# Optimization experiments

Hardware: AMD Instinct MI355X
Metric: run time of the kernel (lower is better)

The kernel has to match this reference:

```python
import jax, jax.numpy as jnp
import numpy as np

T, B, D, H, L = 512, 64, 1024, 1024, 2
W_SCALE = 0.02  # keep tanh out of saturation


def setup_inputs() -> dict:
    key = jax.random.key(0)
    ks = jax.random.split(key, 7)
    return {
        "x": jax.random.normal(ks[0], (T, B, D), dtype=jnp.float32),
        "Wi": jax.random.normal(ks[1], (L, H, D), dtype=jnp.float32) * W_SCALE,
        "bi": jax.random.normal(ks[2], (L, H), dtype=jnp.float32) * W_SCALE,
        "Wh": jax.random.normal(ks[3], (L, H, H), dtype=jnp.float32) * W_SCALE,
        "bh": jax.random.normal(ks[4], (L, H), dtype=jnp.float32) * W_SCALE,
        "Wo": jax.random.normal(ks[5], (L, H, H), dtype=jnp.float32) * W_SCALE,
        "bo": jax.random.normal(ks[6], (L, H), dtype=jnp.float32) * W_SCALE,
    }


def reference(x, Wi, bi, Wh, bh, Wo, bo):
    # Faithful to the original: ONE hidden state shared across all layers,
    # overwritten by each RNNCell call within a timestep.
    num_layers = Wi.shape[0]
    batch = x.shape[1]
    hidden0 = jnp.zeros((batch, Wh.shape[-1]), dtype=x.dtype)

    def step(hidden, xt):
        out = xt
        for l in range(num_layers):
            # h = i2h(out) + h2h(hidden); o = h2o(h); new hidden = tanh(h)
            h = out @ Wi[l].T + bi[l] + hidden @ Wh[l].T + bh[l]  # [B,H]
            out = h @ Wo[l].T + bo[l]
            hidden = jnp.tanh(h)
        return hidden, out

    final_hidden, outs = jax.lax.scan(step, hidden0, x)  # outs: [T,B,H]
    return outs, final_hidden
```

## Files before the change

### kernel.cpp

```cpp
#include <hip/hip_runtime.h>
#include <cstdint>
#include <cstddef>

#define TT   512
#define NWG  256
#define SLOT 65536
#define SLOTB 262144
#define FINALOFF ((size_t)TT * (size_t)SLOT)

#define OFF_M     0
#define OFF_H0    2097152
#define OFF_H1    (OFF_H0 + 131072)
#define OFF_C1    (OFF_H1 + 131072)
#define OFF_FLAGS (OFF_C1 + 4096)

typedef _Float16 f16;
typedef unsigned long long ull;
typedef _Float16 v8h __attribute__((ext_vector_type(8)));
typedef float v4f __attribute__((ext_vector_type(4)));

union U2 { ull u[2]; v8h v; };

__device__ __forceinline__ void st8(void* p, ull v) {
  __hip_atomic_store((ull*)p, v, __ATOMIC_RELAXED, __HIP_MEMORY_SCOPE_AGENT);
}
__device__ __forceinline__ ull ld8(const void* p) {
  return __hip_atomic_load((const ull*)p, __ATOMIC_RELAXED, __HIP_MEMORY_SCOPE_AGENT);
}

__device__ __forceinline__ float rcpf(float x) {
#if __has_builtin(__builtin_amdgcn_rcpf)
  return __builtin_amdgcn_rcpf(x);
#else
  return 1.0f / x;
#endif
}
__device__ __forceinline__ float tanhfast(float x) {
  x = fminf(fmaxf(x, -20.0f), 20.0f);
  const float u = __expf(-2.0f * x);
  return 1.0f - 2.0f * u * rcpf(1.0f + u);
}
__device__ __forceinline__ v8h tanh8(v8h h) {
  v8h r;
#pragma unroll
  for (int i = 0; i < 8; ++i) r[i] = (f16)tanhfast((float)h[i]);
  return r;
}

__global__ void k_init(unsigned int* flags) {
  flags[threadIdx.x] = 0u;
}

__global__ void k_bias_c1(const float* __restrict__ Wi, const float* __restrict__ bi,
                          const float* __restrict__ bh, const float* __restrict__ bo,
                          float* __restrict__ c1) {
  const int i = blockIdx.x * 256 + threadIdx.x;
  const float* row = Wi + 1048576 + (size_t)i * 1024;
  float s = 0.f;
  for (int k = 0; k < 1024; k += 4) {
    const float4 w = *(const float4*)&row[k];
    const float4 v = *(const float4*)&bo[k];
    s += w.x * v.x + w.y * v.y + w.z * v.z + w.w * v.w;
  }
  c1[i] = s + bi[1024 + i] + bh[1024 + i];
}

__global__ __launch_bounds__(256) void k_gemm_M(const float* __restrict__ Wi,
                                                const float* __restrict__ Wo,
                                                f16* __restrict__ Mh) {
  const float* A = Wi + 1048576;
  const float* B = Wo;
  __shared__ float As[16][68];
  __shared__ float Bs[16][68];
  const int bi = blockIdx.x >> 4, bj = blockIdx.x & 15;
  const int i0 = bi * 64, d0 = bj * 64;
  const int ti = threadIdx.x >> 4, tj = threadIdx.x & 15;
  float acc[4][4] = {};
  for (int kc = 0; kc < 1024; kc += 16) {
    const int r = threadIdx.x >> 2, cg = (threadIdx.x & 3) << 2;
    const float4 av = *(const float4*)&A[(size_t)(i0 + r) * 1024 + kc + cg];
    As[cg + 0][r] = av.x; As[cg + 1][r] = av.y; As[cg + 2][r] = av.z; As[cg + 3][r] = av.w;
    const int c2 = threadIdx.x >> 4, dg = (threadIdx.x & 15) << 2;
    const float4 bv = *(const float4*)&B[(size_t)(kc + c2) * 1024 + d0 + dg];
    *(float4*)&Bs[c2][dg] = bv;
    __syncthreads();
#pragma unroll
    for (int kk = 0; kk < 16; ++kk) {
      float a[4], b[4];
#pragma unroll
      for (int q = 0; q < 4; ++q) { a[q] = As[kk][ti * 4 + q]; b[q] = Bs[kk][tj * 4 + q]; }
#pragma unroll
      for (int p = 0; p < 4; ++p)
#pragma unroll
        for (int q = 0; q < 4; ++q) acc[p][q] += a[p] * b[q];
    }
    __syncthreads();
  }
#pragma unroll
  for (int p = 0; p < 4; ++p)
#pragma unroll
    for (int q = 0; q < 4; ++q)
      Mh[(size_t)(i0 + ti * 4 + p) * 1024 + (size_t)(d0 + tj * 4 + q)] = (f16)acc[p][q];
}

__global__ void k_convert_x(const float* __restrict__ x, float* __restrict__ dout) {
  const size_t idx4 = (size_t)blockIdx.x * 256 + threadIdx.x;
  const int t = (int)(idx4 >> 14);
  const int r = (int)(idx4 & 16383);
  const float4 v = ((const float4*)x)[idx4];
  f16* dst = (f16*)((char*)dout + (size_t)t * SLOTB + 131072) + (size_t)r * 4;
  dst[0] = (f16)v.x; dst[1] = (f16)v.y; dst[2] = (f16)v.z; dst[3] = (f16)v.w;
}

__global__ __launch_bounds__(256) void k_z1(const float* __restrict__ Wi,
                                            const float* __restrict__ bi,
                                            const float* __restrict__ bh,
                                            float* __restrict__ dout) {
  const int t = blockIdx.x >> 4, jt = blockIdx.x & 15;
  const int tid = threadIdx.x, l = tid & 63, w = tid >> 6;
  const int lj = l & 15, lk = l >> 4;
  const int jrow = jt * 64 + w * 16 + lj;
  const f16* xh = (const f16*)((const char*)dout + (size_t)t * SLOTB + 131072);
  v4f acc[4] = {{0.f,0.f,0.f,0.f},{0.f,0.f,0.f,0.f},{0.f,0.f,0.f,0.f},{0.f,0.f,0.f,0.f}};
  const float* wrow = Wi + (size_t)jrow * 1024;
  for (int ks = 0; ks < 32; ++ks) {
    const int k0 = ks * 32 + lk * 8;
    const float4 wa = *(const float4*)&wrow[k0];
    const float4 wb = *(const float4*)&wrow[k0 + 4];
    const v8h bf = {(f16)wa.x,(f16)wa.y,(f16)wa.z,(f16)wa.w,
                    (f16)wb.x,(f16)wb.y,(f16)wb.z,(f16)wb.w};
#pragma unroll
    for (int bt = 0; bt < 4; ++bt) {
      const v8h af = *(const v8h*)&xh[(size_t)(bt * 16 + lj) * 1024 + k0];
      acc[bt] = __builtin_amdgcn_mfma_f32_16x16x32_f16(af, bf, acc[bt], 0, 0, 0);
    }
  }
  const float bias = bi[jrow] + bh[jrow];
  f16* z = (f16*)((char*)dout + (size_t)t * SLOTB);
#pragma unroll
  for (int bt = 0; bt < 4; ++bt)
#pragma unroll
    for (int q = 0; q < 4; ++q)
      z[(size_t)(bt * 16 + lk * 4 + q) * 1024 + jrow] = (f16)(acc[bt][q] + bias);
}

__device__ __forceinline__ void gbar_arrive(unsigned int* flags, int wg, unsigned int ph) {
  asm volatile("s_waitcnt vmcnt(0)" ::: "memory");
  __syncthreads();
  if (threadIdx.x == 0)
    __hip_atomic_store(&flags[wg], ph, __ATOMIC_RELAXED, __HIP_MEMORY_SCOPE_AGENT);
}
__device__ __forceinline__ void gbar_wait(unsigned int* flags, unsigned int* gen,
                                          int wg, unsigned int ph) {
  if (wg == 0) {
    const int tt = threadIdx.x;
    if (tt > 0 && tt < NWG)
      while (__hip_atomic_load(&flags[tt], __ATOMIC_RELAXED, __HIP_MEMORY_SCOPE_AGENT) < ph)
        __builtin_amdgcn_s_sleep(1);
    __syncthreads();
    if (tt == 0)
      __hip_atomic_store(gen, ph, __ATOMIC_RELAXED, __HIP_MEMORY_SCOPE_AGENT);
  } else {
    if (threadIdx.x == 0)
      while (__hip_atomic_load(gen, __ATOMIC_RELAXED, __HIP_MEMORY_SCOPE_AGENT) < ph)
        __builtin_amdgcn_s_sleep(1);
    __syncthreads();
  }
  asm volatile("" ::: "memory");
}

__global__ __launch_bounds__(256, 1) void k_rnn(
    const float* __restrict__ Wh, const float* __restrict__ Wo,
    const float* __restrict__ bo,
    char* __restrict__ ws, float* __restrict__ dout)
{
  const f16* Mh = (const f16*)(ws + OFF_M);
  f16* h0h = (f16*)(ws + OFF_H0);
  f16* h1h = (f16*)(ws + OFF_H1);
  const float* c1p = (const float*)(ws + OFF_C1);
  unsigned int* flags = (unsigned int*)(ws + OFF_FLAGS);
  unsigned int* gen = flags + 320;

  const int wg = blockIdx.x;
  const int bq = wg & 3;
  const int jt = wg >> 2;
  const int j0 = jt * 16;
  const int tid = threadIdx.x;
  const int l = tid & 63, w = tid >> 6;
  const int lj = l & 15, lk = l >> 4;
  const int jrow = j0 + lj;

  __shared__ float red[1024];
  __shared__ f16 trh[256];
  __shared__ float trf[256];

  v8h wWh0[8], wM[8], wWh1[8], wWo1[8];
#pragma unroll
  for (int s = 0; s < 8; ++s) {
    const int k0 = w * 256 + s * 32 + lk * 8;
    {
      const float* p = &Wh[(size_t)jrow * 1024 + k0];
      float4 a = *(const float4*)p, b = *(const float4*)(p + 4);
      wWh0[s] = (v8h){(f16)a.x,(f16)a.y,(f16)a.z,(f16)a.w,(f16)b.x,(f16)b.y,(f16)b.z,(f16)b.w};
    }
    {
      const float* p = &Wh[1048576 + (size_t)jrow * 1024 + k0];
      float4 a = *(const float4*)p, b = *(const float4*)(p + 4);
      wWh1[s] = (v8h){(f16)a.x,(f16)a.y,(f16)a.z,(f16)a.w,(f16)b.x,(f16)b.y,(f16)b.z,(f16)b.w};
    }
    {
      const float* p = &Wo[1048576 + (size_t)jrow * 1024 + k0];
      float4 a = *(const float4*)p, b = *(const float4*)(p + 4);
      wWo1[s] = (v8h){(f16)a.x,(f16)a.y,(f16)a.z,(f16)a.w,(f16)b.x,(f16)b.y,(f16)b.z,(f16)b.w};
    }
    wM[s] = *(const v8h*)&Mh[(size_t)jrow * 1024 + k0];
  }
  const int rb = tid >> 4, rj = tid & 15;
  const float c1v = c1p[j0 + rj];
  const float bo1v = bo[1024 + j0 + rj];

  const size_t actbase = (size_t)(bq * 16 + lj) * 1024 + (size_t)(w * 256 + lk * 8);
  unsigned int ph = 0;

  for (int t = 0; t <= TT; ++t) {
    const bool A = (t < TT), R = (t > 0);
    v8h hraw[8];

    if (R) {
      ull u0[8], u1[8];
#pragma unroll
      for (int s = 0; s < 8; ++s) {
        const f16* p = h1h + actbase + s * 32;
        u0[s] = ld8(p); u1[s] = ld8(p + 4);
      }
#pragma unroll
      for (int s = 0; s < 8; ++s) { U2 c; c.u[0] = u0[s]; c.u[1] = u1[s]; hraw[s] = c.v; }
    }

    if (A) {
      v4f acc = {0.f, 0.f, 0.f, 0.f};
      if (R) {
#pragma unroll
        for (int s = 0; s < 8; ++s)
          acc = __builtin_amdgcn_mfma_f32_16x16x32_f16(tanh8(hraw[s]), wWh0[s], acc, 0, 0, 0);
      }
#pragma unroll
      for (int q = 0; q < 4; ++q) red[w * 256 + (lk * 4 + q) * 16 + lj] = acc[q];
      __syncthreads();
      float h0 = red[tid] + red[256 + tid] + red[512 + tid] + red[768 + tid];
      const f16* z1 = (const f16*)((const char*)dout + (size_t)t * SLOTB);
      h0 += (float)z1[(size_t)(bq * 16 + rb) * 1024 + j0 + rj];
      trh[tid] = (f16)h0;
      __syncthreads();
      if (tid < 64)
        st8(&h0h[(size_t)(bq * 16 + (tid >> 2)) * 1024 + j0 + (tid & 3) * 4],
            ((const ull*)trh)[tid]);
    }
    gbar_arrive(flags, wg, ++ph);

    if (R) {
      v4f a2 = {0.f, 0.f, 0.f, 0.f};
#pragma unroll
      for (int s = 0; s < 8; ++s)
        a2 = __builtin_amdgcn_mfma_f32_16x16x32_f16(hraw[s], wWo1[s], a2, 0, 0, 0);
#pragma unroll
      for (int q = 0; q < 4; ++q) red[w * 256 + (lk * 4 + q) * 16 + lj] = a2[q];
      __syncthreads();
      trf[tid] = red[tid] + red[256 + tid] + red[512 + tid] + red[768 + tid] + bo1v;
      __syncthreads();
      if (tid < 128)
        st8(&dout[(size_t)(t - 1) * SLOT + (size_t)(bq * 16 + (tid >> 3)) * 1024 + j0 + (tid & 7) * 2],
            ((const ull*)trf)[tid]);
    }
    gbar_wait(flags, gen, wg, ph);

    if (A) {
      ull g0[8], g1[8];
#pragma unroll
      for (int s = 0; s < 8; ++s) {
        const f16* p = h0h + actbase + s * 32;
        g0[s] = ld8(p); g1[s] = ld8(p + 4);
      }
      v4f aM = {0.f, 0.f, 0.f, 0.f}, aW = {0.f, 0.f, 0.f, 0.f};
#pragma unroll
      for (int s = 0; s < 8; ++s) {
        U2 c; c.u[0] = g0[s]; c.u[1] = g1[s];
        const v8h gv = c.v;
        aM = __builtin_amdgcn_mfma_f32_16x16x32_f16(gv, wM[s], aM, 0, 0, 0);
        aW = __builtin_amdgcn_mfma_f32_16x16x32_f16(tanh8(gv), wWh1[s], aW, 0, 0, 0);
      }
#pragma unroll
      for (int q = 0; q < 4; ++q) red[w * 256 + (lk * 4 + q) * 16 + lj] = aM[q] + aW[q];
      __syncthreads();
      const float h1 = red[tid] + red[256 + tid] + red[512 + tid] + red[768 + tid] + c1v;
      trh[tid] = (f16)h1;
      const bool last = (t == TT - 1);
      if (last) trf[tid] = tanhfast(h1);
      __syncthreads();
      if (tid < 64)
        st8(&h1h[(size_t)(bq * 16 + (tid >> 2)) * 1024 + j0 + (tid & 3) * 4],
            ((const ull*)trh)[tid]);
      if (last && tid < 128)
        st8(&dout[FINALOFF + (size_t)(bq * 16 + (tid >> 3)) * 1024 + j0 + (tid & 7) * 2],
            ((const ull*)trf)[tid]);
      gbar_arrive(flags, wg, ++ph);
      gbar_wait(flags, gen, wg, ph);
    }
  }
}

extern "C" void kernel_launch(void* const* d_in, const int* in_sizes, int n_in,
                              void* d_out, int out_size, void* d_ws, size_t ws_size,
                              hipStream_t stream) {
  (void)in_sizes; (void)n_in; (void)out_size; (void)ws_size;
  const float* x  = (const float*)d_in[0];
  const float* Wi = (const float*)d_in[1];
  const float* bi = (const float*)d_in[2];
  const float* Wh = (const float*)d_in[3];
  const float* bh = (const float*)d_in[4];
  const float* Wo = (const float*)d_in[5];
  const float* bo = (const float*)d_in[6];
  char* ws = (char*)d_ws;
  float* out = (float*)d_out;

  k_init<<<1, 512, 0, stream>>>((unsigned int*)(ws + OFF_FLAGS));
  k_convert_x<<<32768, 256, 0, stream>>>(x, out);
  k_bias_c1<<<4, 256, 0, stream>>>(Wi, bi, bh, bo, (float*)(ws + OFF_C1));
  k_gemm_M<<<256, 256, 0, stream>>>(Wi, Wo, (f16*)(ws + OFF_M));
  k_z1<<<8192, 256, 0, stream>>>(Wi, bi, bh, out);
  k_rnn<<<NWG, 256, 0, stream>>>(Wh, Wo, bo, ws, out);
}
```

Baseline: 6.034 ms.

## Fuse layer-0 input projection into persistent RNN kernel and localize barriers

Removes the separate x conversion and z1 GEMM kernels. Each workgroup now caches its Wi slice in LDS as fp16 and computes the next timestep's input projection while waiting at the barrier. The global barrier changes from one master workgroup gathering all flags to independent 64-workgroup groups per batch quarter, each polling its peers directly. Tanh of each hidden state is computed once by its producer and stored alongside it, so consumers no longer recompute tanh8. The cost is extra LDS, extra global stores per step, and more barrier polling traffic.

```diff
diff --git a/kernel.cpp b/kernel.cpp
--- a/kernel.cpp
+++ b/kernel.cpp
@@ -5,13 +5,15 @@
 #define TT   512
 #define NWG  256
 #define SLOT 65536
-#define SLOTB 262144
 #define FINALOFF ((size_t)TT * (size_t)SLOT)
 
 #define OFF_M     0
 #define OFF_H0    2097152
-#define OFF_H1    (OFF_H0 + 131072)
-#define OFF_C1    (OFF_H1 + 131072)
+#define OFF_TH0   (OFF_H0 + 131072)
+#define OFF_H1    (OFF_TH0 + 131072)
+#define OFF_TH1   (OFF_H1 + 131072)
+#define OFF_B0    (OFF_TH1 + 131072)
+#define OFF_C1    (OFF_B0 + 4096)
 #define OFF_FLAGS (OFF_C1 + 4096)
 
 typedef _Float16 f16;
@@ -40,20 +42,14 @@
   const float u = __expf(-2.0f * x);
   return 1.0f - 2.0f * u * rcpf(1.0f + u);
 }
-__device__ __forceinline__ v8h tanh8(v8h h) {
-  v8h r;
-#pragma unroll
-  for (int i = 0; i < 8; ++i) r[i] = (f16)tanhfast((float)h[i]);
-  return r;
-}
 
 __global__ void k_init(unsigned int* flags) {
   flags[threadIdx.x] = 0u;
 }
 
-__global__ void k_bias_c1(const float* __restrict__ Wi, const float* __restrict__ bi,
-                          const float* __restrict__ bh, const float* __restrict__ bo,
-                          float* __restrict__ c1) {
+__global__ void k_bias(const float* __restrict__ Wi, const float* __restrict__ bi,
+                       const float* __restrict__ bh, const float* __restrict__ bo,
+                       float* __restrict__ b0, float* __restrict__ c1) {
   const int i = blockIdx.x * 256 + threadIdx.x;
   const float* row = Wi + 1048576 + (size_t)i * 1024;
   float s = 0.f;
@@ -63,6 +59,7 @@
     s += w.x * v.x + w.y * v.y + w.z * v.z + w.w * v.w;
   }
   c1[i] = s + bi[1024 + i] + bh[1024 + i];
+  b0[i] = bi[i] + bh[i];
 }
 
 __global__ __launch_bounds__(256) void k_gemm_M(const float* __restrict__ Wi,
@@ -103,83 +100,42 @@
       Mh[(size_t)(i0 + ti * 4 + p) * 1024 + (size_t)(d0 + tj * 4 + q)] = (f16)acc[p][q];
 }
 
-__global__ void k_convert_x(const float* __restrict__ x, float* __restrict__ dout) {
-  const size_t idx4 = (size_t)blockIdx.x * 256 + threadIdx.x;
-  const int t = (int)(idx4 >> 14);
-  const int r = (int)(idx4 & 16383);
-  const float4 v = ((const float4*)x)[idx4];
-  f16* dst = (f16*)((char*)dout + (size_t)t * SLOTB + 131072) + (size_t)r * 4;
-  dst[0] = (f16)v.x; dst[1] = (f16)v.y; dst[2] = (f16)v.z; dst[3] = (f16)v.w;
-}
-
-__global__ __launch_bounds__(256) void k_z1(const float* __restrict__ Wi,
-                                            const float* __restrict__ bi,
-                                            const float* __restrict__ bh,
-                                            float* __restrict__ dout) {
-  const int t = blockIdx.x >> 4, jt = blockIdx.x & 15;
-  const int tid = threadIdx.x, l = tid & 63, w = tid >> 6;
-  const int lj = l & 15, lk = l >> 4;
-  const int jrow = jt * 64 + w * 16 + lj;
-  const f16* xh = (const f16*)((const char*)dout + (size_t)t * SLOTB + 131072);
-  v4f acc[4] = {{0.f,0.f,0.f,0.f},{0.f,0.f,0.f,0.f},{0.f,0.f,0.f,0.f},{0.f,0.f,0.f,0.f}};
-  const float* wrow = Wi + (size_t)jrow * 1024;
-  for (int ks = 0; ks < 32; ++ks) {
-    const int k0 = ks * 32 + lk * 8;
-    const float4 wa = *(const float4*)&wrow[k0];
-    const float4 wb = *(const float4*)&wrow[k0 + 4];
-    const v8h bf = {(f16)wa.x,(f16)wa.y,(f16)wa.z,(f16)wa.w,
-                    (f16)wb.x,(f16)wb.y,(f16)wb.z,(f16)wb.w};
-#pragma unroll
-    for (int bt = 0; bt < 4; ++bt) {
-      const v8h af = *(const v8h*)&xh[(size_t)(bt * 16 + lj) * 1024 + k0];
-      acc[bt] = __builtin_amdgcn_mfma_f32_16x16x32_f16(af, bf, acc[bt], 0, 0, 0);
-    }
-  }
-  const float bias = bi[jrow] + bh[jrow];
-  f16* z = (f16*)((char*)dout + (size_t)t * SLOTB);
-#pragma unroll
-  for (int bt = 0; bt < 4; ++bt)
-#pragma unroll
-    for (int q = 0; q < 4; ++q)
-      z[(size_t)(bt * 16 + lk * 4 + q) * 1024 + jrow] = (f16)(acc[bt][q] + bias);
-}
-
-__device__ __forceinline__ void gbar_arrive(unsigned int* flags, int wg, unsigned int ph) {
+__device__ __forceinline__ void gbar_arrive(unsigned int* gf, int slot, unsigned int ph) {
   asm volatile("s_waitcnt vmcnt(0)" ::: "memory");
   __syncthreads();
   if (threadIdx.x == 0)
-    __hip_atomic_store(&flags[wg], ph, __ATOMIC_RELAXED, __HIP_MEMORY_SCOPE_AGENT);
-}
-__device__ __forceinline__ void gbar_wait(unsigned int* flags, unsigned int* gen,
-                                          int wg, unsigned int ph) {
-  if (wg == 0) {
-    const int tt = threadIdx.x;
-    if (tt > 0 && tt < NWG)
-      while (__hip_atomic_load(&flags[tt], __ATOMIC_RELAXED, __HIP_MEMORY_SCOPE_AGENT) < ph)
-        __builtin_amdgcn_s_sleep(1);
-    __syncthreads();
-    if (tt == 0)
-      __hip_atomic_store(gen, ph, __ATOMIC_RELAXED, __HIP_MEMORY_SCOPE_AGENT);
-  } else {
-    if (threadIdx.x == 0)
-      while (__hip_atomic_load(gen, __ATOMIC_RELAXED, __HIP_MEMORY_SCOPE_AGENT) < ph)
-        __builtin_amdgcn_s_sleep(1);
-    __syncthreads();
-  }
+    __hip_atomic_store(&gf[slot * 4], ph, __ATOMIC_RELAXED, __HIP_MEMORY_SCOPE_AGENT);
+}
+__device__ __forceinline__ void gbar_wait(unsigned int* gf, unsigned int ph) {
+  if (threadIdx.x < 64)
+    while (__hip_atomic_load(&gf[threadIdx.x * 4], __ATOMIC_RELAXED, __HIP_MEMORY_SCOPE_AGENT) < ph)
+      __builtin_amdgcn_s_sleep(1);
+  __syncthreads();
   asm volatile("" ::: "memory");
 }
 
+__device__ __forceinline__ void ld_frags(const f16* base, v8h out[8]) {
+  ull u0[8], u1[8];
+#pragma unroll
+  for (int s = 0; s < 8; ++s) { const f16* p = base + s * 32; u0[s] = ld8(p); u1[s] = ld8(p + 4); }
+#pragma unroll
+  for (int s = 0; s < 8; ++s) { U2 c; c.u[0] = u0[s]; c.u[1] = u1[s]; out[s] = c.v; }
+}
+
 __global__ __launch_bounds__(256, 1) void k_rnn(
-    const float* __restrict__ Wh, const float* __restrict__ Wo,
-    const float* __restrict__ bo,
+    const float* __restrict__ x,
+    const float* __restrict__ Wi, const float* __restrict__ Wh,
+    const float* __restrict__ Wo, const float* __restrict__ bo,
     char* __restrict__ ws, float* __restrict__ dout)
 {
-  const f16* Mh = (const f16*)(ws + OFF_M);
-  f16* h0h = (f16*)(ws + OFF_H0);
-  f16* h1h = (f16*)(ws + OFF_H1);
+  const f16* Mh  = (const f16*)(ws + OFF_M);
+  f16* h0h  = (f16*)(ws + OFF_H0);
+  f16* th0h = (f16*)(ws + OFF_TH0);
+  f16* h1h  = (f16*)(ws + OFF_H1);
+  f16* th1h = (f16*)(ws + OFF_TH1);
+  const float* b0p = (const float*)(ws + OFF_B0);
   const float* c1p = (const float*)(ws + OFF_C1);
   unsigned int* flags = (unsigned int*)(ws + OFF_FLAGS);
-  unsigned int* gen = flags + 320;
 
   const int wg = blockIdx.x;
   const int bq = wg & 3;
@@ -189,9 +145,12 @@
   const int l = tid & 63, w = tid >> 6;
   const int lj = l & 15, lk = l >> 4;
   const int jrow = j0 + lj;
-
+  unsigned int* gf = flags + bq * 256;
+
+  __shared__ __align__(16) f16 WiL[16 * 1032];
   __shared__ float red[1024];
   __shared__ f16 trh[256];
+  __shared__ f16 trh2[256];
   __shared__ float trf[256];
 
   v8h wWh0[8], wM[8], wWh1[8], wWo1[8];
@@ -215,56 +174,89 @@
     }
     wM[s] = *(const v8h*)&Mh[(size_t)jrow * 1024 + k0];
   }
-  const int rb = tid >> 4, rj = tid & 15;
+  for (int u = tid; u < 4096; u += 256) {
+    const int rr = u >> 8, c4 = (u & 255) << 2;
+    const float4 v = *(const float4*)&Wi[(size_t)(j0 + rr) * 1024 + c4];
+    f16* dst = &WiL[rr * 1032 + c4];
+    dst[0] = (f16)v.x; dst[1] = (f16)v.y; dst[2] = (f16)v.z; dst[3] = (f16)v.w;
+  }
+  const int rj = tid & 15;
+  const float b0v = b0p[j0 + rj];
   const float c1v = c1p[j0 + rj];
   const float bo1v = bo[1024 + j0 + rj];
+  __syncthreads();
 
   const size_t actbase = (size_t)(bq * 16 + lj) * 1024 + (size_t)(w * 256 + lk * 8);
+  const int redw = w * 256 + lk * 64 + lj;
+
+  auto z1_dot = [&](const float* xt) -> float {
+    v4f acc = {0.f, 0.f, 0.f, 0.f};
+#pragma unroll
+    for (int s = 0; s < 8; ++s) {
+      const float* p = xt + actbase + s * 32;
+      const float4 a = *(const float4*)p;
+      const float4 b = *(const float4*)(p + 4);
+      const v8h af = {(f16)a.x,(f16)a.y,(f16)a.z,(f16)a.w,
+                      (f16)b.x,(f16)b.y,(f16)b.z,(f16)b.w};
+      const v8h bf = *(const v8h*)&WiL[lj * 1032 + w * 256 + s * 32 + lk * 8];
+      acc = __builtin_amdgcn_mfma_f32_16x16x32_f16(af, bf, acc, 0, 0, 0);
+    }
+#pragma unroll
+    for (int q = 0; q < 4; ++q) red[redw + q * 16] = acc[q];
+    __syncthreads();
+    const float r = red[tid] + red[256 + tid] + red[512 + tid] + red[768 + tid] + b0v;
+    __syncthreads();
+    return r;
+  };
+
+  float zc = z1_dot(x);
   unsigned int ph = 0;
 
   for (int t = 0; t <= TT; ++t) {
     const bool A = (t < TT), R = (t > 0);
-    v8h hraw[8];
+    v8h thf[8], hrf[8];
 
     if (R) {
-      ull u0[8], u1[8];
-#pragma unroll
-      for (int s = 0; s < 8; ++s) {
-        const f16* p = h1h + actbase + s * 32;
-        u0[s] = ld8(p); u1[s] = ld8(p + 4);
-      }
-#pragma unroll
-      for (int s = 0; s < 8; ++s) { U2 c; c.u[0] = u0[s]; c.u[1] = u1[s]; hraw[s] = c.v; }
-    }
-
-    if (A) {
+      ld_frags(th1h + actbase, thf);
+      ld_frags(h1h + actbase, hrf);
+    }
+
+    {
       v4f acc = {0.f, 0.f, 0.f, 0.f};
       if (R) {
 #pragma unroll
         for (int s = 0; s < 8; ++s)
-          acc = __builtin_amdgcn_mfma_f32_16x16x32_f16(tanh8(hraw[s]), wWh0[s], acc, 0, 0, 0);
-      }
-#pragma unroll
-      for (int q = 0; q < 4; ++q) red[w * 256 + (lk * 4 + q) * 16 + lj] = acc[q];
-      __syncthreads();
-      float h0 = red[tid] + red[256 + tid] + red[512 + tid] + red[768 + tid];
-      const f16* z1 = (const f16*)((const char*)dout + (size_t)t * SLOTB);
-      h0 += (float)z1[(size_t)(bq * 16 + rb) * 1024 + j0 + rj];
-      trh[tid] = (f16)h0;
-      __syncthreads();
-      if (tid < 64)
-        st8(&h0h[(size_t)(bq * 16 + (tid >> 2)) * 1024 + j0 + (tid & 3) * 4],
-            ((const ull*)trh)[tid]);
-    }
-    gbar_arrive(flags, wg, ++ph);
+          acc = __builtin_amdgcn_mfma_f32_16x16x32_f16(thf[s], wWh0[s], acc, 0, 0, 0);
+      }
+#pragma unroll
+      for (int q = 0; q < 4; ++q) red[redw + q * 16] = acc[q];
+      __syncthreads();
+      if (A) {
+        const float h0 = red[tid] + red[256 + tid] + red[512 + tid] + red[768 + tid] + zc;
+        trh[tid] = (f16)h0;
+        trh2[tid] = (f16)tanhfast(h0);
+      }
+      __syncthreads();
+      if (A) {
+        if (tid < 64) {
+          st8(&h0h[(size_t)(bq * 16 + (tid >> 2)) * 1024 + j0 + (tid & 3) * 4],
+              ((const ull*)trh)[tid]);
+        } else if (tid < 128) {
+          const int u = tid - 64;
+          st8(&th0h[(size_t)(bq * 16 + (u >> 2)) * 1024 + j0 + (u & 3) * 4],
+              ((const ull*)trh2)[u]);
+        }
+      }
+    }
+    gbar_arrive(gf, jt, ++ph);
 
     if (R) {
       v4f a2 = {0.f, 0.f, 0.f, 0.f};
 #pragma unroll
       for (int s = 0; s < 8; ++s)
-        a2 = __builtin_amdgcn_mfma_f32_16x16x32_f16(hraw[s], wWo1[s], a2, 0, 0, 0);
-#pragma unroll
-      for (int q = 0; q < 4; ++q) red[w * 256 + (lk * 4 + q) * 16 + lj] = a2[q];
+        a2 = __builtin_amdgcn_mfma_f32_16x16x32_f16(hrf[s], wWo1[s], a2, 0, 0, 0);
+#pragma unroll
+      for (int q = 0; q < 4; ++q) red[redw + q * 16] = a2[q];
       __syncthreads();
       trf[tid] = red[tid] + red[256 + tid] + red[512 + tid] + red[768 + tid] + bo1v;
       __syncthreads();
@@ -272,39 +264,46 @@
         st8(&dout[(size_t)(t - 1) * SLOT + (size_t)(bq * 16 + (tid >> 3)) * 1024 + j0 + (tid & 7) * 2],
             ((const ull*)trf)[tid]);
     }
-    gbar_wait(flags, gen, wg, ph);
+    gbar_wait(gf, ph);
 
     if (A) {
-      ull g0[8], g1[8];
+      v8h g0f[8], t0f[8];
+      ld_frags(h0h + actbase, g0f);
+      ld_frags(th0h + actbase, t0f);
+      v4f aM = {0.f, 0.f, 0.f, 0.f}, aW = {0.f, 0.f, 0.f, 0.f};
 #pragma unroll
       for (int s = 0; s < 8; ++s) {
-        const f16* p = h0h + actbase + s * 32;
-        g0[s] = ld8(p); g1[s] = ld8(p + 4);
-      }
-      v4f aM = {0.f, 0.f, 0.f, 0.f}, aW = {0.f, 0.f, 0.f, 0.f};
-#pragma unroll
-      for (int s = 0; s < 8; ++s) {
-        U2 c; c.u[0] = g0[s]; c.u[1] = g1[s];
-        const v8h gv = c.v;
-        aM = __builtin_amdgcn_mfma_f32_16x16x32_f16(gv, wM[s], aM, 0, 0, 0);
-        aW = __builtin_amdgcn_mfma_f32_16x16x32_f16(tanh8(gv), wWh1[s], aW, 0, 0, 0);
-      }
-#pragma unroll
-      for (int q = 0; q < 4; ++q) red[w * 256 + (lk * 4 + q) * 16 + lj] = aM[q] + aW[q];
+        aM = __builtin_amdgcn_mfma_f32_16x16x32_f16(g0f[s], wM[s], aM, 0, 0, 0);
+        aW = __builtin_amdgcn_mfma_f32_16x16x32_f16(t0f[s], wWh1[s], aW, 0, 0, 0);
+      }
+#pragma unroll
+      for (int q = 0; q < 4; ++q) red[redw + q * 16] = aM[q] + aW[q];
       __syncthreads();
       const float h1 = red[tid] + red[256 + tid] + red[512 + tid] + red[768 + tid] + c1v;
+      const bool last = (t == TT - 1);
       trh[tid] = (f16)h1;
-      const bool last = (t == TT - 1);
-      if (last) trf[tid] = tanhfast(h1);
-      __syncthreads();
-      if (tid < 64)
+      const float th1v = tanhfast(h1);
+      trh2[tid] = (f16)th1v;
+      if (last) trf[tid] = th1v;
+      __syncthreads();
+      if (tid < 64) {
         st8(&h1h[(size_t)(bq * 16 + (tid >> 2)) * 1024 + j0 + (tid & 3) * 4],
             ((const ull*)trh)[tid]);
+      } else if (tid < 128) {
+        const int u = tid - 64;
+        st8(&th1h[(size_t)(bq * 16 + (u >> 2)) * 1024 + j0 + (u & 3) * 4],
+            ((const ull*)trh2)[u]);
+      }
       if (last && tid < 128)
         st8(&dout[FINALOFF + (size_t)(bq * 16 + (tid >> 3)) * 1024 + j0 + (tid & 7) * 2],
             ((const ull*)trf)[tid]);
-      gbar_arrive(flags, wg, ++ph);
-      gbar_wait(flags, gen, wg, ph);
+      gbar_arrive(gf, jt, ++ph);
+
+      float zn = zc;
+      if (t + 1 < TT)
+        zn = z1_dot(x + (size_t)(t + 1) * SLOT);
+      gbar_wait(gf, ph);
+      zc = zn;
     }
   }
 }
@@ -323,10 +322,8 @@
   char* ws = (char*)d_ws;
   float* out = (float*)d_out;
 
-  k_init<<<1, 512, 0, stream>>>((unsigned int*)(ws + OFF_FLAGS));
-  k_convert_x<<<32768, 256, 0, stream>>>(x, out);
-  k_bias_c1<<<4, 256, 0, stream>>>(Wi, bi, bh, bo, (float*)(ws + OFF_C1));
+  k_init<<<1, 1024, 0, stream>>>((unsigned int*)(ws + OFF_FLAGS));
+  k_bias<<<4, 256, 0, stream>>>(Wi, bi, bh, bo, (float*)(ws + OFF_B0), (float*)(ws + OFF_C1));
   k_gemm_M<<<256, 256, 0, stream>>>(Wi, Wo, (f16*)(ws + OFF_M));
-  k_z1<<<8192, 256, 0, stream>>>(Wi, bi, bh, out);
-  k_rnn<<<NWG, 256, 0, stream>>>(Wh, Wo, bo, ws, out);
-}
+  k_rnn<<<NWG, 256, 0, stream>>>(x, Wi, Wh, Wo, bo, ws, out);
+}
```

Measured after the change: 6.767 ms. 1.12x slower.
